# Performance work log

Measured on AMD Instinct MI355X. Metric: run time of the kernel, lower is better.

## Reference

```python
import jax, jax.numpy as jnp
import numpy as np

NUM_HEADS = 16
EPS = 1e-5
CHUNK = 128  # chunk length for the chunked recurrent-state scan


def _linear_attention(x, Wq, Wk, Wv, Wo, bo):
    B, T, E = x.shape
    H = NUM_HEADS
    d = E // H

    def proj(W):
        # nn.Linear(bias=False): y = x @ W.T ; split heads -> (B,H,T,d)
        return (x @ W.T).reshape(B, T, H, d).transpose(0, 2, 1, 3)

    phi_q = jax.nn.elu(proj(Wq)) + 1.0
    phi_k = jax.nn.elu(proj(Wk)) + 1.0
    V = proj(Wv)

    nC = T // CHUNK
    # (nC, B, H, C, d) so lax.scan iterates over chunks of time
    def to_chunks(a):
        return a.reshape(B, H, nC, CHUNK, d).transpose(2, 0, 1, 3, 4)

    qc, kc, vc = to_chunks(phi_q), to_chunks(phi_k), to_chunks(V)
    mask = jnp.tril(jnp.ones((CHUNK, CHUNK), x.dtype))  # causal incl. diagonal

    S0 = jnp.zeros((B, H, d, d), x.dtype)  # running sum of k v^T
    z0 = jnp.zeros((B, H, d), x.dtype)     # running sum of phi_k

    def step(carry, inp):
        S, z = carry
        q, k, v = inp  # (B,H,C,d)
        A = jnp.einsum('bhid,bhjd->bhij', q, k) * mask
        num = jnp.einsum('bhij,bhjd->bhid', A, v) + jnp.einsum('bhid,bhde->bhie', q, S)
        den = jnp.sum(A, axis=-1) + jnp.einsum('bhid,bhd->bhi', q, z) + EPS
        out = num / den[..., None]
        S = S + jnp.einsum('bhjd,bhje->bhde', k, v)
        z = z + jnp.sum(k, axis=2)
        return (S, z), out

    _, outs = jax.lax.scan(step, (S0, z0), (qc, kc, vc))  # (nC,B,H,C,d)
    out = outs.transpose(1, 2, 0, 3, 4).reshape(B, H, T, d)
    out = out.transpose(0, 2, 1, 3).reshape(B, T, E)
    # out_proj (dropout p=0 / eval -> identity)
    return out @ Wo.T + bo


def setup_inputs() -> dict:
    key = jax.random.key(0)
    ks = jax.random.split(key, 6)
    B, T, E = 2, 2048, 1024
    s = 1.0 / np.sqrt(E)
    return {
        'x': jax.random.normal(ks[0], (B, T, E), jnp.float32),
        'Wq': jax.random.normal(ks[1], (E, E), jnp.float32) * s,
        'Wk': jax.random.normal(ks[2], (E, E), jnp.float32) * s,
        'Wv': jax.random.normal(ks[3], (E, E), jnp.float32) * s,
        'Wo': jax.random.normal(ks[4], (E, E), jnp.float32) * s,
        'bo': jnp.zeros((E,), jnp.float32),
    }


def reference(x, Wq, Wk, Wv, Wo, bo):
    return _linear_attention(x, Wq, Wk, Wv, Wo, bo)
```

## Files before the change

### kernel.cpp

```cpp
#include <hip/hip_runtime.h>
#include <hip/hip_bf16.h>
#include <stdint.h>

typedef __attribute__((ext_vector_type(4))) float  floatx4;
typedef __attribute__((ext_vector_type(8))) short  short8;
typedef __attribute__((ext_vector_type(8))) unsigned short ushortx8;
typedef __attribute__((ext_vector_type(4))) unsigned short ushortx4;

#define B_  2
#define T_  2048
#define E_  1024
#define H_  16
#define D_  64
#define C_  128
#define NC_ 16
#define M_  4096
#define EPS_ 1e-5f

__device__ __forceinline__ unsigned short f2b(float f) {
    union { float f; unsigned int u; } v; v.f = f;
    unsigned int r = v.u + 0x7fffu + ((v.u >> 16) & 1u);
    return (unsigned short)(r >> 16);
}
__device__ __forceinline__ float b2f(unsigned short b) {
    union { unsigned int u; float f; } v; v.u = ((unsigned int)b) << 16;
    return v.f;
}

__device__ __forceinline__ int stage_seg(int i) { return (i & 3) ^ ((i >> 3) & 3); }
__device__ __forceinline__ int frag_slot(int lane) {
    int m = lane & 15, q = lane >> 4;
    return m * 4 + (q ^ ((m >> 1) & 3));
}

__global__ __launch_bounds__(256) void convert_all(const float* __restrict__ x,
                                                   const float* __restrict__ Wq,
                                                   const float* __restrict__ Wk,
                                                   const float* __restrict__ Wv,
                                                   const float* __restrict__ Wo,
                                                   unsigned short* __restrict__ dst) {
    int i = (blockIdx.x * 256 + threadIdx.x) * 4;
    const float* s; int off;
    if (i < M_ * E_) { s = x; off = i; }
    else {
        int j = i - M_ * E_;
        int which = j >> 20;
        s = (which == 0) ? Wq : (which == 1) ? Wk : (which == 2) ? Wv : Wo;
        off = j & ((1 << 20) - 1);
    }
    float4 f = *(const float4*)(s + off);
    ushortx4 o;
    o[0] = f2b(f.x); o[1] = f2b(f.y); o[2] = f2b(f.z); o[3] = f2b(f.w);
    *(ushortx4*)(dst + i) = o;
}

__global__ __launch_bounds__(256) void gemm_qkv(const unsigned short* __restrict__ A,
                                                const unsigned short* __restrict__ Bm,
                                                unsigned short* __restrict__ Cb) {
    const int N = 3 * E_, K = E_;
    __shared__ __align__(16) unsigned short at[8 * 512];
    __shared__ __align__(16) unsigned short bt[16 * 512];
    int tid = threadIdx.x;
    int wave = tid >> 6, lane = tid & 63;
    int wr = wave >> 1, wc = wave & 1;
    int m = lane & 15, q = lane >> 4;
    int srow = lane >> 2, sseg = stage_seg(lane);
    int fs = frag_slot(lane);
    int row0 = blockIdx.y * 64, col0 = blockIdx.x * 128;
    floatx4 acc[2][4];
    for (int i = 0; i < 2; i++) for (int j = 0; j < 4; j++) acc[i][j] = floatx4{0.f, 0.f, 0.f, 0.f};

    for (int k0 = 0; k0 < K; k0 += 64) {
        __syncthreads();
        for (int p = 0; p < 2; p++) {
            int t = p * 4 + wave;
            int rt = t & 3, kh = t >> 2;
            const unsigned short* ga = A + (size_t)(row0 + rt * 16 + srow) * K + k0 + kh * 32 + sseg * 8;
            __builtin_amdgcn_global_load_lds((const __attribute__((address_space(1))) unsigned int*)ga,
                (__attribute__((address_space(3))) unsigned int*)(at + t * 512), 16, 0, 0);
        }
        for (int p = 0; p < 4; p++) {
            int t = p * 4 + wave;
            int rt = t & 7, kh = t >> 3;
            const unsigned short* gb = Bm + (size_t)(col0 + rt * 16 + srow) * K + k0 + kh * 32 + sseg * 8;
            __builtin_amdgcn_global_load_lds((const __attribute__((address_space(1))) unsigned int*)gb,
                (__attribute__((address_space(3))) unsigned int*)(bt + t * 512), 16, 0, 0);
        }
        __syncthreads();
        for (int kh = 0; kh < 2; kh++) {
            short8 af[2], bfr[4];
            for (int mi = 0; mi < 2; mi++) af[mi]  = *(const short8*)(at + (kh * 4 + wr * 2 + mi) * 512 + fs * 8);
            for (int ni = 0; ni < 4; ni++) bfr[ni] = *(const short8*)(bt + (kh * 8 + wc * 4 + ni) * 512 + fs * 8);
            for (int mi = 0; mi < 2; mi++)
                for (int ni = 0; ni < 4; ni++)
                    acc[mi][ni] = __builtin_amdgcn_mfma_f32_16x16x32_bf16(af[mi], bfr[ni], acc[mi][ni], 0, 0, 0);
        }
    }
    int qrow = q * 4;
    for (int mi = 0; mi < 2; mi++) for (int ni = 0; ni < 4; ni++) {
        int col = col0 + wc * 64 + ni * 16 + m;
        bool isphi = (col < 2 * E_);
        for (int r2 = 0; r2 < 4; r2++) {
            int row = row0 + wr * 32 + mi * 16 + qrow + r2;
            float v = acc[mi][ni][r2];
            if (isphi) v = (v > 0.f) ? (v + 1.f) : __expf(v);
            Cb[(size_t)row * N + col] = f2b(v);
        }
    }
}

__global__ __launch_bounds__(256) void gemm_out(const unsigned short* __restrict__ A,
                                                const unsigned short* __restrict__ Bm,
                                                const float* __restrict__ bias,
                                                float* __restrict__ Cf) {
    const int N = E_, K = E_;
    __shared__ __align__(16) unsigned short at[8 * 512];
    __shared__ __align__(16) unsigned short bt[8 * 512];
    int tid = threadIdx.x;
    int wave = tid >> 6, lane = tid & 63;
    int wr = wave >> 1, wc = wave & 1;
    int m = lane & 15, q = lane >> 4;
    int srow = lane >> 2, sseg = stage_seg(lane);
    int fs = frag_slot(lane);
    int row0 = blockIdx.y * 64, col0 = blockIdx.x * 64;
    floatx4 acc[2][2];
    for (int i = 0; i < 2; i++) for (int j = 0; j < 2; j++) acc[i][j] = floatx4{0.f, 0.f, 0.f, 0.f};

    for (int k0 = 0; k0 < K; k0 += 64) {
        __syncthreads();
        for (int p = 0; p < 2; p++) {
            int t = p * 4 + wave;
            int rt = t & 3, kh = t >> 2;
            const unsigned short* ga = A  + (size_t)(row0 + rt * 16 + srow) * K + k0 + kh * 32 + sseg * 8;
            const unsigned short* gb = Bm + (size_t)(col0 + rt * 16 + srow) * K + k0 + kh * 32 + sseg * 8;
            __builtin_amdgcn_global_load_lds((const __attribute__((address_space(1))) unsigned int*)ga,
                (__attribute__((address_space(3))) unsigned int*)(at + t * 512), 16, 0, 0);
            __builtin_amdgcn_global_load_lds((const __attribute__((address_space(1))) unsigned int*)gb,
                (__attribute__((address_space(3))) unsigned int*)(bt + t * 512), 16, 0, 0);
        }
        __syncthreads();
        for (int kh = 0; kh < 2; kh++) {
            short8 af[2], bfr[2];
            for (int mi = 0; mi < 2; mi++) af[mi]  = *(const short8*)(at + (kh * 4 + wr * 2 + mi) * 512 + fs * 8);
            for (int ci = 0; ci < 2; ci++) bfr[ci] = *(const short8*)(bt + (kh * 4 + wc * 2 + ci) * 512 + fs * 8);
            for (int mi = 0; mi < 2; mi++)
                for (int ci = 0; ci < 2; ci++)
                    acc[mi][ci] = __builtin_amdgcn_mfma_f32_16x16x32_bf16(af[mi], bfr[ci], acc[mi][ci], 0, 0, 0);
        }
    }
    int qrow = q * 4;
    for (int ci = 0; ci < 2; ci++) {
        int col = col0 + wc * 32 + ci * 16 + m;
        float bv = bias[col];
        for (int mi = 0; mi < 2; mi++)
            for (int r2 = 0; r2 < 4; r2++) {
                int row = row0 + wr * 32 + mi * 16 + qrow + r2;
                Cf[(size_t)row * N + col] = acc[mi][ci][r2] + bv;
            }
    }
}

__global__ __launch_bounds__(256) void chunk_sums(const unsigned short* __restrict__ qkv,
                                                  float* __restrict__ Sc, float* __restrict__ zc) {
    int c = blockIdx.x, h = blockIdx.y, bb = blockIdx.z;
    __shared__ __align__(16) unsigned short Kt[64 * 132];
    __shared__ __align__(16) unsigned short Vt[80 * 132];
    int tid = threadIdx.x;
    int lane = tid & 63, w = tid >> 6;
    size_t rowb = (size_t)bb * T_ + (size_t)c * C_;
    int kcol = E_ + h * D_, vcol = 2 * E_ + h * D_;

    for (int s = 0; s < 4; s++) {
        int off = s * 256 + tid;
        int r = off >> 3, seg = (off & 7) * 8;
        size_t g = (rowb + r) * 3072;
        ushortx8 k8 = *(const ushortx8*)(qkv + g + kcol + seg);
        ushortx8 v8 = *(const ushortx8*)(qkv + g + vcol + seg);
        for (int e = 0; e < 8; e++) {
            Kt[(seg + e) * 132 + r] = k8[e];
            Vt[(seg + e) * 132 + r] = v8[e];
        }
    }
    if (tid < 128) Vt[64 * 132 + tid] = 0x3f80;
    __syncthreads();

    floatx4 acc[5];
    for (int ni = 0; ni < 5; ni++) acc[ni] = floatx4{0.f, 0.f, 0.f, 0.f};
    int lm = lane & 15, lk = (lane >> 4) * 8;
    for (int k0 = 0; k0 < 128; k0 += 32) {
        short8 af = *(const short8*)(Kt + (w * 16 + lm) * 132 + k0 + lk);
        for (int ni = 0; ni < 5; ni++) {
            short8 bf = *(const short8*)(Vt + (ni * 16 + lm) * 132 + k0 + lk);
            acc[ni] = __builtin_amdgcn_mfma_f32_16x16x32_bf16(af, bf, acc[ni], 0, 0, 0);
        }
    }
    size_t base = ((size_t)(bb * H_ + h) * NC_ + c) * (size_t)(D_ * D_);
    int r0 = w * 16 + (lane >> 4) * 4;
    for (int ni = 0; ni < 4; ni++)
        for (int reg = 0; reg < 4; reg++)
            Sc[base + (size_t)(r0 + reg) * D_ + ni * 16 + lm] = acc[ni][reg];
    if (lm == 0) {
        size_t zb = ((size_t)(bb * H_ + h) * NC_ + c) * D_;
        for (int reg = 0; reg < 4; reg++) zc[zb + r0 + reg] = acc[4][reg];
    }
}

__global__ __launch_bounds__(256) void attn_kernel(const unsigned short* __restrict__ qkv,
                                                   const float* __restrict__ Sc,
                                                   const float* __restrict__ zc,
                                                   unsigned short* __restrict__ attn) {
    int c = blockIdx.x, h = blockIdx.y, bb = blockIdx.z;
    __shared__ __align__(16) unsigned short qs[128 * 68];
    __shared__ __align__(16) unsigned short ks[128 * 68];
    __shared__ __align__(16) unsigned short vt[64 * 132];
    __shared__ __align__(16) unsigned short ovl[128 * 36];
    __shared__ float zsh[64];
    int tid = threadIdx.x;
    int lane = tid & 63, w = tid >> 6;
    int lm = lane & 15, lq = lane >> 4;
    size_t rowb = (size_t)bb * T_ + (size_t)c * C_;
    int qcol = h * D_, kcol = E_ + h * D_, vcol = 2 * E_ + h * D_;

    for (int s = 0; s < 4; s++) {
        int off = s * 256 + tid;
        int r = off >> 3, seg = (off & 7) * 8;
        size_t g = (rowb + r) * 3072;
        ushortx8 q8 = *(const ushortx8*)(qkv + g + qcol + seg);
        ushortx8 k8 = *(const ushortx8*)(qkv + g + kcol + seg);
        ushortx8 v8 = *(const ushortx8*)(qkv + g + vcol + seg);
        *(ushortx8*)(qs + r * 68 + seg) = q8;
        *(ushortx8*)(ks + r * 68 + seg) = k8;
        for (int e = 0; e < 8; e++) vt[(seg + e) * 132 + r] = v8[e];
    }
    {
        size_t scb = ((size_t)(bb * H_ + h) * NC_) * (size_t)(D_ * D_);
        int p = tid * 16;
        float a[16];
        for (int i = 0; i < 16; i++) a[i] = 0.f;
        for (int j = 0; j < c; j++) {
            const float* Sj = Sc + scb + (size_t)j * (D_ * D_) + p;
            for (int q = 0; q < 16; q += 4) {
                float4 f = *(const float4*)(Sj + q);
                a[q] += f.x; a[q + 1] += f.y; a[q + 2] += f.z; a[q + 3] += f.w;
            }
        }
        for (int i = 0; i < 16; i++) {
            int d = (p + i) >> 6, e = (p + i) & 63;
            ovl[e * 68 + d] = f2b(a[i]);
        }
    }
    if (tid < 64) {
        size_t zb = ((size_t)(bb * H_ + h) * NC_) * D_;
        float zr = 0.f;
        for (int j = 0; j < c; j++) zr += zc[zb + (size_t)j * D_ + tid];
        zsh[tid] = zr;
    }
    __syncthreads();

    floatx4 acc[2][4];
    for (int mi = 0; mi < 2; mi++) for (int ni = 0; ni < 4; ni++) acc[mi][ni] = floatx4{0.f, 0.f, 0.f, 0.f};
    for (int k0 = 0; k0 < 64; k0 += 32) {
        short8 aq[2];
        for (int mi = 0; mi < 2; mi++)
            aq[mi] = *(const short8*)(qs + (w * 32 + mi * 16 + lm) * 68 + k0 + lq * 8);
        for (int ni = 0; ni < 4; ni++) {
            short8 bs = *(const short8*)(ovl + (ni * 16 + lm) * 68 + k0 + lq * 8);
            for (int mi = 0; mi < 2; mi++)
                acc[mi][ni] = __builtin_amdgcn_mfma_f32_16x16x32_bf16(aq[mi], bs, acc[mi][ni], 0, 0, 0);
        }
    }
    float dsum[2][4];
    {
        int d0 = lm * 4;
        float4 z4 = *(const float4*)(zsh + d0);
        for (int mi = 0; mi < 2; mi++)
            for (int reg = 0; reg < 4; reg++) {
                int row = w * 32 + mi * 16 + lq * 4 + reg;
                ushortx4 q4 = *(const ushortx4*)(qs + row * 68 + d0);
                dsum[mi][reg] = b2f(q4[0]) * z4.x + b2f(q4[1]) * z4.y + b2f(q4[2]) * z4.z + b2f(q4[3]) * z4.w;
            }
    }
    __syncthreads();

    for (int jt = 0; jt <= w; jt++) {
        floatx4 pa[2][2];
        for (int mi = 0; mi < 2; mi++) for (int ct = 0; ct < 2; ct++) pa[mi][ct] = floatx4{0.f, 0.f, 0.f, 0.f};
        for (int k0 = 0; k0 < 64; k0 += 32) {
            short8 aq[2];
            for (int mi = 0; mi < 2; mi++)
                aq[mi] = *(const short8*)(qs + (w * 32 + mi * 16 + lm) * 68 + k0 + lq * 8);
            for (int ct = 0; ct < 2; ct++) {
                short8 bk = *(const short8*)(ks + (jt * 32 + ct * 16 + lm) * 68 + k0 + lq * 8);
                for (int mi = 0; mi < 2; mi++)
                    pa[mi][ct] = __builtin_amdgcn_mfma_f32_16x16x32_bf16(aq[mi], bk, pa[mi][ct], 0, 0, 0);
            }
        }
        bool diag = (jt == w);
        for (int mi = 0; mi < 2; mi++)
            for (int ct = 0; ct < 2; ct++)
                for (int reg = 0; reg < 4; reg++) {
                    int il = mi * 16 + lq * 4 + reg;
                    int jl = ct * 16 + lm;
                    float v = pa[mi][ct][reg];
                    if (diag && jl > il) v = 0.f;
                    dsum[mi][reg] += v;
                    ovl[(w * 32 + il) * 36 + jl] = f2b(v);
                }
        short8 ap[2];
        for (int mi = 0; mi < 2; mi++)
            ap[mi] = *(const short8*)(ovl + (w * 32 + mi * 16 + lm) * 36 + lq * 8);
        for (int ni = 0; ni < 4; ni++) {
            short8 bv = *(const short8*)(vt + (ni * 16 + lm) * 132 + jt * 32 + lq * 8);
            for (int mi = 0; mi < 2; mi++)
                acc[mi][ni] = __builtin_amdgcn_mfma_f32_16x16x32_bf16(ap[mi], bv, acc[mi][ni], 0, 0, 0);
        }
    }

    for (int off = 1; off < 16; off <<= 1)
        for (int mi = 0; mi < 2; mi++)
            for (int reg = 0; reg < 4; reg++)
                dsum[mi][reg] += __shfl_xor(dsum[mi][reg], off);

    for (int mi = 0; mi < 2; mi++)
        for (int reg = 0; reg < 4; reg++) {
            float inv = 1.f / (dsum[mi][reg] + EPS_);
            int row = w * 32 + mi * 16 + lq * 4 + reg;
            for (int ni = 0; ni < 4; ni++)
                attn[(rowb + row) * E_ + h * D_ + ni * 16 + lm] = f2b(acc[mi][ni][reg] * inv);
        }
}

extern "C" void kernel_launch(void* const* d_in, const int* in_sizes, int n_in,
                              void* d_out, int out_size, void* d_ws, size_t ws_size,
                              hipStream_t stream) {
    const float* x  = (const float*)d_in[0];
    const float* Wq = (const float*)d_in[1];
    const float* Wk = (const float*)d_in[2];
    const float* Wv = (const float*)d_in[3];
    const float* Wo = (const float*)d_in[4];
    const float* bo = (const float*)d_in[5];
    float* out = (float*)d_out;

    const size_t MB = 1024 * 1024;
    uint8_t* ws = (uint8_t*)d_ws;
    unsigned short* xb    = (unsigned short*)(ws + 0);
    unsigned short* wb    = (unsigned short*)(ws + 8 * MB);
    unsigned short* wob   = wb + 3 * E_ * E_;
    unsigned short* qkvb  = (unsigned short*)(ws + 16 * MB);
    float* Sc = (float*)(ws + 40 * MB);
    float* zc = (float*)(ws + 48 * MB);
    unsigned short* attnb = xb;

    convert_all<<<(M_ * E_ + 4 * E_ * E_) / 1024, 256, 0, stream>>>(x, Wq, Wk, Wv, Wo, xb);

    gemm_qkv<<<dim3(24, 64), 256, 0, stream>>>(xb, wb, qkvb);
    chunk_sums<<<dim3(NC_, H_, B_), 256, 0, stream>>>(qkvb, Sc, zc);
    attn_kernel<<<dim3(NC_, H_, B_), 256, 0, stream>>>(qkvb, Sc, zc, attnb);
    gemm_out<<<dim3(16, 64), 256, 0, stream>>>(attnb, wob, bo, out);
}
```

Baseline: 166.2 us.

## Switch QKV GEMM to 32x32x16 MFMA with two-wave blocks

Rewrites the QKV projection GEMM to use 32x32x16 bf16 MFMA instructions instead of 16x16x32. It halves the block to 128 threads, each wave computing a 64x64 tile, and reworks fragment addressing and the epilogue row mapping to match. The goal is fewer LDS fragment reads per MFMA and higher per-wave compute density. The cost is half as many waves per block for latency hiding and more accumulator registers per thread.

```diff
diff --git a/kernel.cpp b/kernel.cpp
--- a/kernel.cpp
+++ b/kernel.cpp
@@ -2,10 +2,11 @@
 #include <hip/hip_bf16.h>
 #include <stdint.h>
 
-typedef __attribute__((ext_vector_type(4))) float  floatx4;
-typedef __attribute__((ext_vector_type(8))) short  short8;
-typedef __attribute__((ext_vector_type(8))) unsigned short ushortx8;
-typedef __attribute__((ext_vector_type(4))) unsigned short ushortx4;
+typedef __attribute__((ext_vector_type(4)))  float  floatx4;
+typedef __attribute__((ext_vector_type(16))) float  floatx16;
+typedef __attribute__((ext_vector_type(8)))  short  short8;
+typedef __attribute__((ext_vector_type(8)))  unsigned short ushortx8;
+typedef __attribute__((ext_vector_type(4)))  unsigned short ushortx4;
 
 #define B_  2
 #define T_  2048
@@ -28,9 +29,9 @@
 }
 
 __device__ __forceinline__ int stage_seg(int i) { return (i & 3) ^ ((i >> 3) & 3); }
+__device__ __forceinline__ int sigma_slot(int r, int s) { return r * 4 + (s ^ ((r >> 1) & 3)); }
 __device__ __forceinline__ int frag_slot(int lane) {
-    int m = lane & 15, q = lane >> 4;
-    return m * 4 + (q ^ ((m >> 1) & 3));
+    return sigma_slot(lane & 15, lane >> 4);
 }
 
 __global__ __launch_bounds__(256) void convert_all(const float* __restrict__ x,
@@ -54,59 +55,68 @@
     *(ushortx4*)(dst + i) = o;
 }
 
-__global__ __launch_bounds__(256) void gemm_qkv(const unsigned short* __restrict__ A,
+__global__ __launch_bounds__(128) void gemm_qkv(const unsigned short* __restrict__ A,
                                                 const unsigned short* __restrict__ Bm,
                                                 unsigned short* __restrict__ Cb) {
     const int N = 3 * E_, K = E_;
     __shared__ __align__(16) unsigned short at[8 * 512];
     __shared__ __align__(16) unsigned short bt[16 * 512];
     int tid = threadIdx.x;
-    int wave = tid >> 6, lane = tid & 63;
-    int wr = wave >> 1, wc = wave & 1;
-    int m = lane & 15, q = lane >> 4;
+    int w = tid >> 6, lane = tid & 63;
+    int l31 = lane & 31, lh = lane >> 5;
     int srow = lane >> 2, sseg = stage_seg(lane);
-    int fs = frag_slot(lane);
     int row0 = blockIdx.y * 64, col0 = blockIdx.x * 128;
-    floatx4 acc[2][4];
-    for (int i = 0; i < 2; i++) for (int j = 0; j < 4; j++) acc[i][j] = floatx4{0.f, 0.f, 0.f, 0.f};
+    floatx16 acc[2][2];
+    for (int i = 0; i < 2; i++) for (int j = 0; j < 2; j++)
+        for (int r = 0; r < 16; r++) acc[i][j][r] = 0.f;
+
+    int am[2], bn[2];
+    for (int mi = 0; mi < 2; mi++) am[mi] = mi * 32 + l31;
+    for (int nj = 0; nj < 2; nj++) bn[nj] = w * 64 + nj * 32 + l31;
 
     for (int k0 = 0; k0 < K; k0 += 64) {
         __syncthreads();
-        for (int p = 0; p < 2; p++) {
-            int t = p * 4 + wave;
-            int rt = t & 3, kh = t >> 2;
-            const unsigned short* ga = A + (size_t)(row0 + rt * 16 + srow) * K + k0 + kh * 32 + sseg * 8;
+        for (int p = 0; p < 4; p++) {
+            int t = w * 4 + p;
+            const unsigned short* ga = A + (size_t)(row0 + (t & 3) * 16 + srow) * K + k0 + (t >> 2) * 32 + sseg * 8;
             __builtin_amdgcn_global_load_lds((const __attribute__((address_space(1))) unsigned int*)ga,
                 (__attribute__((address_space(3))) unsigned int*)(at + t * 512), 16, 0, 0);
         }
-        for (int p = 0; p < 4; p++) {
-            int t = p * 4 + wave;
-            int rt = t & 7, kh = t >> 3;
-            const unsigned short* gb = Bm + (size_t)(col0 + rt * 16 + srow) * K + k0 + kh * 32 + sseg * 8;
+        for (int p = 0; p < 8; p++) {
+            int u = w * 8 + p;
+            const unsigned short* gb = Bm + (size_t)(col0 + (u & 7) * 16 + srow) * K + k0 + (u >> 3) * 32 + sseg * 8;
             __builtin_amdgcn_global_load_lds((const __attribute__((address_space(1))) unsigned int*)gb,
-                (__attribute__((address_space(3))) unsigned int*)(bt + t * 512), 16, 0, 0);
+                (__attribute__((address_space(3))) unsigned int*)(bt + u * 512), 16, 0, 0);
         }
         __syncthreads();
-        for (int kh = 0; kh < 2; kh++) {
-            short8 af[2], bfr[4];
-            for (int mi = 0; mi < 2; mi++) af[mi]  = *(const short8*)(at + (kh * 4 + wr * 2 + mi) * 512 + fs * 8);
-            for (int ni = 0; ni < 4; ni++) bfr[ni] = *(const short8*)(bt + (kh * 8 + wc * 4 + ni) * 512 + fs * 8);
-            for (int mi = 0; mi < 2; mi++)
-                for (int ni = 0; ni < 4; ni++)
-                    acc[mi][ni] = __builtin_amdgcn_mfma_f32_16x16x32_bf16(af[mi], bfr[ni], acc[mi][ni], 0, 0, 0);
-        }
-    }
-    int qrow = q * 4;
-    for (int mi = 0; mi < 2; mi++) for (int ni = 0; ni < 4; ni++) {
-        int col = col0 + wc * 64 + ni * 16 + m;
-        bool isphi = (col < 2 * E_);
-        for (int r2 = 0; r2 < 4; r2++) {
-            int row = row0 + wr * 32 + mi * 16 + qrow + r2;
-            float v = acc[mi][ni][r2];
-            if (isphi) v = (v > 0.f) ? (v + 1.f) : __expf(v);
-            Cb[(size_t)row * N + col] = f2b(v);
-        }
-    }
+        for (int ks = 0; ks < 4; ks++) {
+            int kh = ks >> 1;
+            int s = (ks & 1) * 2 + lh;
+            short8 af[2], bf[2];
+            for (int mi = 0; mi < 2; mi++) {
+                int m = am[mi];
+                af[mi] = *(const short8*)(at + (kh * 4 + (m >> 4)) * 512 + sigma_slot(m & 15, s) * 8);
+            }
+            for (int nj = 0; nj < 2; nj++) {
+                int n = bn[nj];
+                bf[nj] = *(const short8*)(bt + (kh * 8 + (n >> 4)) * 512 + sigma_slot(n & 15, s) * 8);
+            }
+            for (int mi = 0; mi < 2; mi++)
+                for (int nj = 0; nj < 2; nj++)
+                    acc[mi][nj] = __builtin_amdgcn_mfma_f32_32x32x16_bf16(af[mi], bf[nj], acc[mi][nj], 0, 0, 0);
+        }
+    }
+    for (int mi = 0; mi < 2; mi++)
+        for (int nj = 0; nj < 2; nj++) {
+            int col = col0 + w * 64 + nj * 32 + l31;
+            bool isphi = (col < 2 * E_);
+            for (int reg = 0; reg < 16; reg++) {
+                int row = row0 + mi * 32 + (reg & 3) + 8 * (reg >> 2) + 4 * lh;
+                float v = acc[mi][nj][reg];
+                if (isphi) v = (v > 0.f) ? (v + 1.f) : __expf(v);
+                Cb[(size_t)row * N + col] = f2b(v);
+            }
+        }
 }
 
 __global__ __launch_bounds__(256) void gemm_out(const unsigned short* __restrict__ A,
@@ -353,7 +363,7 @@
 
     convert_all<<<(M_ * E_ + 4 * E_ * E_) / 1024, 256, 0, stream>>>(x, Wq, Wk, Wv, Wo, xb);
 
-    gemm_qkv<<<dim3(24, 64), 256, 0, stream>>>(xb, wb, qkvb);
+    gemm_qkv<<<dim3(24, 64), 128, 0, stream>>>(xb, wb, qkvb);
     chunk_sums<<<dim3(NC_, H_, B_), 256, 0, stream>>>(qkvb, Sc, zc);
     attn_kernel<<<dim3(NC_, H_, B_), 256, 0, stream>>>(qkvb, Sc, zc, attnb);
     gemm_out<<<dim3(16, 64), 256, 0, stream>>>(attnb, wob, bo, out);
```

Result: slower. 176.5 us (+6.2%).

## Double-buffer A tiles in LDS and stream B fragments directly from global

Applied to the files above, without the earlier changes.

Both GEMM kernels now keep two LDS buffers for the A tile and prefetch the next k-step while computing the current one, so each iteration needs only one barrier instead of two. The B operand no longer goes through LDS: each lane loads its MFMA fragment straight from global memory using precomputed row pointers. This is meant to cut LDS staging traffic and barrier stalls. In exchange, B loads are strided per lane, less coalesced and exposed to latency with no prefetch. Correctness also relies on the barrier waiting for the async LDS loads to finish.

```diff
diff --git a/kernel.cpp b/kernel.cpp
--- a/kernel.cpp
+++ b/kernel.cpp
@@ -2,10 +2,10 @@
 #include <hip/hip_bf16.h>
 #include <stdint.h>
 
-typedef __attribute__((ext_vector_type(4))) float  floatx4;
-typedef __attribute__((ext_vector_type(8))) short  short8;
-typedef __attribute__((ext_vector_type(8))) unsigned short ushortx8;
-typedef __attribute__((ext_vector_type(4))) unsigned short ushortx4;
+typedef __attribute__((ext_vector_type(4)))  float  floatx4;
+typedef __attribute__((ext_vector_type(8)))  short  short8;
+typedef __attribute__((ext_vector_type(8)))  unsigned short ushortx8;
+typedef __attribute__((ext_vector_type(4)))  unsigned short ushortx4;
 
 #define B_  2
 #define T_  2048
@@ -58,8 +58,7 @@
                                                 const unsigned short* __restrict__ Bm,
                                                 unsigned short* __restrict__ Cb) {
     const int N = 3 * E_, K = E_;
-    __shared__ __align__(16) unsigned short at[8 * 512];
-    __shared__ __align__(16) unsigned short bt[16 * 512];
+    __shared__ __align__(16) unsigned short at[2][8 * 512];
     int tid = threadIdx.x;
     int wave = tid >> 6, lane = tid & 63;
     int wr = wave >> 1, wc = wave & 1;
@@ -70,30 +69,37 @@
     floatx4 acc[2][4];
     for (int i = 0; i < 2; i++) for (int j = 0; j < 4; j++) acc[i][j] = floatx4{0.f, 0.f, 0.f, 0.f};
 
-    for (int k0 = 0; k0 < K; k0 += 64) {
+    const unsigned short* bp[4];
+    for (int ni = 0; ni < 4; ni++)
+        bp[ni] = Bm + (size_t)(col0 + wc * 64 + ni * 16 + m) * K + q * 8;
+
+    for (int p = 0; p < 2; p++) {
+        int t = p * 4 + wave;
+        const unsigned short* ga = A + (size_t)(row0 + (t & 3) * 16 + srow) * K + (t >> 2) * 32 + sseg * 8;
+        __builtin_amdgcn_global_load_lds((const __attribute__((address_space(1))) unsigned int*)ga,
+            (__attribute__((address_space(3))) unsigned int*)(at[0] + t * 512), 16, 0, 0);
+    }
+
+    for (int it = 0; it < 16; it++) {
+        int k0 = it * 64;
         __syncthreads();
+        int kn = (it < 15) ? k0 + 64 : k0;
         for (int p = 0; p < 2; p++) {
             int t = p * 4 + wave;
-            int rt = t & 3, kh = t >> 2;
-            const unsigned short* ga = A + (size_t)(row0 + rt * 16 + srow) * K + k0 + kh * 32 + sseg * 8;
+            const unsigned short* ga = A + (size_t)(row0 + (t & 3) * 16 + srow) * K + kn + (t >> 2) * 32 + sseg * 8;
             __builtin_amdgcn_global_load_lds((const __attribute__((address_space(1))) unsigned int*)ga,
-                (__attribute__((address_space(3))) unsigned int*)(at + t * 512), 16, 0, 0);
-        }
-        for (int p = 0; p < 4; p++) {
-            int t = p * 4 + wave;
-            int rt = t & 7, kh = t >> 3;
-            const unsigned short* gb = Bm + (size_t)(col0 + rt * 16 + srow) * K + k0 + kh * 32 + sseg * 8;
-            __builtin_amdgcn_global_load_lds((const __attribute__((address_space(1))) unsigned int*)gb,
-                (__attribute__((address_space(3))) unsigned int*)(bt + t * 512), 16, 0, 0);
-        }
-        __syncthreads();
+                (__attribute__((address_space(3))) unsigned int*)(at[(it + 1) & 1] + t * 512), 16, 0, 0);
+        }
+        const unsigned short* ab = at[it & 1];
         for (int kh = 0; kh < 2; kh++) {
-            short8 af[2], bfr[4];
-            for (int mi = 0; mi < 2; mi++) af[mi]  = *(const short8*)(at + (kh * 4 + wr * 2 + mi) * 512 + fs * 8);
-            for (int ni = 0; ni < 4; ni++) bfr[ni] = *(const short8*)(bt + (kh * 8 + wc * 4 + ni) * 512 + fs * 8);
+            short8 af[2], bf[4];
+            for (int mi = 0; mi < 2; mi++)
+                af[mi] = *(const short8*)(ab + (kh * 4 + wr * 2 + mi) * 512 + fs * 8);
+            for (int ni = 0; ni < 4; ni++)
+                bf[ni] = *(const short8*)(bp[ni] + k0 + kh * 32);
             for (int mi = 0; mi < 2; mi++)
                 for (int ni = 0; ni < 4; ni++)
-                    acc[mi][ni] = __builtin_amdgcn_mfma_f32_16x16x32_bf16(af[mi], bfr[ni], acc[mi][ni], 0, 0, 0);
+                    acc[mi][ni] = __builtin_amdgcn_mfma_f32_16x16x32_bf16(af[mi], bf[ni], acc[mi][ni], 0, 0, 0);
         }
     }
     int qrow = q * 4;
@@ -114,8 +120,7 @@
                                                 const float* __restrict__ bias,
                                                 float* __restrict__ Cf) {
     const int N = E_, K = E_;
-    __shared__ __align__(16) unsigned short at[8 * 512];
-    __shared__ __align__(16) unsigned short bt[8 * 512];
+    __shared__ __align__(16) unsigned short at[2][8 * 512];
     int tid = threadIdx.x;
     int wave = tid >> 6, lane = tid & 63;
     int wr = wave >> 1, wc = wave & 1;
@@ -126,26 +131,37 @@
     floatx4 acc[2][2];
     for (int i = 0; i < 2; i++) for (int j = 0; j < 2; j++) acc[i][j] = floatx4{0.f, 0.f, 0.f, 0.f};
 
-    for (int k0 = 0; k0 < K; k0 += 64) {
+    const unsigned short* bp[2];
+    for (int ci = 0; ci < 2; ci++)
+        bp[ci] = Bm + (size_t)(col0 + wc * 32 + ci * 16 + m) * K + q * 8;
+
+    for (int p = 0; p < 2; p++) {
+        int t = p * 4 + wave;
+        const unsigned short* ga = A + (size_t)(row0 + (t & 3) * 16 + srow) * K + (t >> 2) * 32 + sseg * 8;
+        __builtin_amdgcn_global_load_lds((const __attribute__((address_space(1))) unsigned int*)ga,
+            (__attribute__((address_space(3))) unsigned int*)(at[0] + t * 512), 16, 0, 0);
+    }
+
+    for (int it = 0; it < 16; it++) {
+        int k0 = it * 64;
         __syncthreads();
+        int kn = (it < 15) ? k0 + 64 : k0;
         for (int p = 0; p < 2; p++) {
             int t = p * 4 + wave;
-            int rt = t & 3, kh = t >> 2;
-            const unsigned short* ga = A  + (size_t)(row0 + rt * 16 + srow) * K + k0 + kh * 32 + sseg * 8;
-            const unsigned short* gb = Bm + (size_t)(col0 + rt * 16 + srow) * K + k0 + kh * 32 + sseg * 8;
+            const unsigned short* ga = A + (size_t)(row0 + (t & 3) * 16 + srow) * K + kn + (t >> 2) * 32 + sseg * 8;
             __builtin_amdgcn_global_load_lds((const __attribute__((address_space(1))) unsigned int*)ga,
-                (__attribute__((address_space(3))) unsigned int*)(at + t * 512), 16, 0, 0);
-            __builtin_amdgcn_global_load_lds((const __attribute__((address_space(1))) unsigned int*)gb,
-                (__attribute__((address_space(3))) unsigned int*)(bt + t * 512), 16, 0, 0);
-        }
-        __syncthreads();
+                (__attribute__((address_space(3))) unsigned int*)(at[(it + 1) & 1] + t * 512), 16, 0, 0);
+        }
+        const unsigned short* ab = at[it & 1];
         for (int kh = 0; kh < 2; kh++) {
-            short8 af[2], bfr[2];
-            for (int mi = 0; mi < 2; mi++) af[mi]  = *(const short8*)(at + (kh * 4 + wr * 2 + mi) * 512 + fs * 8);
-            for (int ci = 0; ci < 2; ci++) bfr[ci] = *(const short8*)(bt + (kh * 4 + wc * 2 + ci) * 512 + fs * 8);
+            short8 af[2], bf[2];
+            for (int mi = 0; mi < 2; mi++)
+                af[mi] = *(const short8*)(ab + (kh * 4 + wr * 2 + mi) * 512 + fs * 8);
+            for (int ci = 0; ci < 2; ci++)
+                bf[ci] = *(const short8*)(bp[ci] + k0 + kh * 32);
             for (int mi = 0; mi < 2; mi++)
                 for (int ci = 0; ci < 2; ci++)
-                    acc[mi][ci] = __builtin_amdgcn_mfma_f32_16x16x32_bf16(af[mi], bfr[ci], acc[mi][ci], 0, 0, 0);
+                    acc[mi][ci] = __builtin_amdgcn_mfma_f32_16x16x32_bf16(af[mi], bf[ci], acc[mi][ci], 0, 0, 0);
         }
     }
     int qrow = q * 4;
```

After: 244.5 us. +47.1%, slower.
